# Optimization experiments

Hardware: AMD Instinct MI355X
Metric: run time of the kernel (lower is better)

## Reference

```python
import jax, jax.numpy as jnp
import numpy as np

N_RADIAL = 5
N_BASIS = 7
R_MAX = 6.0
R_MIN = 0.5
N_SPECIES = 119
N_ATOMS = 50000
N_EDGES = 1000000


def tril_2d_indices(n):
    return np.array([(i, j) for i in range(n) for j in range(i + 1)], dtype=np.int32)


def tril_3d_indices(n):
    return np.array([(i, j, k) for i in range(n) for j in range(i + 1) for k in range(j + 1)], dtype=np.int32)


TRIL2 = tril_2d_indices(N_RADIAL)  # [15, 2]
TRIL3 = tril_3d_indices(N_RADIAL)  # [35, 3]


def setup_inputs() -> dict:
    key = jax.random.key(0)
    k1, k2, k3, k4 = jax.random.split(key, 4)
    R = jax.random.normal(k1, (N_ATOMS, 3), dtype=jnp.float32) * 1.5
    Z = jax.random.randint(k2, (N_ATOMS,), 0, N_SPECIES, dtype=jnp.int32)
    neighbor_idxs = jax.random.randint(k3, (2, N_EDGES), 0, N_ATOMS, dtype=jnp.int32)
    box = jnp.zeros((3,), dtype=jnp.float32)
    W = jax.random.normal(k4, (N_SPECIES, N_SPECIES, N_RADIAL, N_BASIS), dtype=jnp.float32)
    return {"R": R, "Z": Z, "neighbor_idxs": neighbor_idxs, "box": box, "W": W}


def reference(R, Z, neighbor_idxs, box, W):
    n_atoms = R.shape[0]
    idx_i, idx_j = neighbor_idxs[0], neighbor_idxs[1]
    # free-space displacement (init_box == 0): R[idx_j] - R[idx_i]
    dr_vec = (R[idx_j] - R[idx_i]).astype(jnp.float32)  # [E, 3]
    dr = jnp.sqrt(jnp.sum(dr_vec * dr_vec, axis=-1))    # [E]
    dn = dr_vec / (dr + 1e-5)[:, None]                  # unit directions [E, 3]

    # radial function: Gaussian basis * cosine cutoff, species-pair coefficients
    shifts = R_MIN + (R_MAX - R_MIN) / N_BASIS * jnp.arange(N_BASIS, dtype=jnp.float32)
    betta = float(N_BASIS ** 2) / float(R_MAX ** 2)
    rad_norm = float((2.0 * betta / np.pi) ** 0.25)
    basis = rad_norm * jnp.exp(-betta * (dr[:, None] - shifts) ** 2)  # [E, n_basis]
    cutoff = 0.5 * (jnp.cos(np.pi * dr / R_MAX) + 1.0) * (dr < R_MAX).astype(dr.dtype)
    coeffs = W[Z[idx_i], Z[idx_j]]  # [E, n_radial, n_basis]
    embed_norm = float(1.0 / np.sqrt(N_BASIS))
    radial = jnp.einsum('en,ern->er', basis, coeffs) * cutoff[:, None] * embed_norm  # [E, R]

    # mask padded (self-index) neighbors
    radial = radial * (idx_i != idx_j).astype(radial.dtype)[:, None]

    # geometric moments: scatter-add per-edge rank-0..3 outer products onto atoms
    seg = lambda x: jax.ops.segment_sum(x, idx_j, num_segments=n_atoms)
    m0 = seg(radial)                                           # [A, R]
    m1 = seg(radial[:, :, None] * dn[:, None, :])              # [A, R, 3]
    dn2 = dn[:, None, :, None] * dn[:, None, None, :]          # [E, 1, 3, 3]
    m2 = seg(radial[:, :, None, None] * dn2)                   # [A, R, 3, 3]
    dn3 = dn2[..., None] * dn[:, None, None, None, :]          # [E, 1, 3, 3, 3]
    m3 = seg(radial[:, :, None, None, None] * dn3)             # [A, R, 3, 3, 3]

    contr_0 = m0
    contr_1 = jnp.einsum('ari,asi->rsa', m1, m1)
    contr_2 = jnp.einsum('arij,asij->rsa', m2, m2)
    contr_3 = jnp.einsum('arijk,asijk->rsa', m3, m3)
    contr_4 = jnp.einsum('arij,asik,atjk->rsta', m2, m2, m2)
    contr_5 = jnp.einsum('ari,asj,atij->rsta', m1, m1, m2)
    contr_6 = jnp.einsum('arijk,asijl,atkl->rsta', m3, m3, m2)
    contr_7 = jnp.einsum('arijk,asij,atk->rsta', m3, m2, m1)

    i2, j2 = TRIL2[:, 0], TRIL2[:, 1]
    i3, j3, k3 = TRIL3[:, 0], TRIL3[:, 1], TRIL3[:, 2]
    n_symm01 = TRIL2.shape[0] * N_RADIAL  # 75

    c1 = jnp.transpose(contr_1[i2, j2])                                    # [A, 15]
    c2 = jnp.transpose(contr_2[i2, j2])                                    # [A, 15]
    c3 = jnp.transpose(contr_3[i2, j2])                                    # [A, 15]
    c4 = jnp.transpose(contr_4[i3, j3, k3])                                # [A, 35]
    c5 = jnp.transpose(jnp.reshape(contr_5[i2, j2], (n_symm01, -1)))       # [A, 75]
    c6 = jnp.transpose(jnp.reshape(contr_6[i2, j2], (n_symm01, -1)))       # [A, 75]
    c7 = jnp.transpose(jnp.reshape(contr_7, (N_RADIAL ** 3, -1)))          # [A, 125]

    return jnp.concatenate([contr_0, c1, c2, c3, c4, c5, c6, c7], axis=-1)  # [A, 360]
```

## Files before the change

kernel.cpp:

```cpp
#include <hip/hip_runtime.h>
#include <cstdint>
#include <cstddef>

#define CAP 48
#define NSP 119
#define CPAD 16

__device__ constexpr int IDX2[9]  = {0,1,2, 1,3,4, 2,4,5};
__device__ constexpr int IDX3[27] = {0,1,2, 1,3,4, 2,4,5,
                                     1,3,4, 3,6,7, 4,7,8,
                                     2,4,5, 4,7,8, 5,8,9};
__device__ constexpr int PR2[15] = {0,1,1,2,2,2,3,3,3,3,4,4,4,4,4};
__device__ constexpr int PS2[15] = {0,0,1,0,1,2,0,1,2,3,0,1,2,3,4};
__device__ constexpr int CB4[15] = {50,51,52,54,55,57,60,61,63,66,70,71,73,76,80};

__global__ __launch_bounds__(256) void prep_kernel(
    const float* __restrict__ R, const int* __restrict__ Z,
    const float* __restrict__ W,
    int* __restrict__ cnt, float4* __restrict__ RZ, float* __restrict__ Wp,
    int n_atoms, int n_wel)
{
    int t = blockIdx.x * blockDim.x + threadIdx.x;
    if (t < n_atoms) {
        cnt[t * CPAD] = 0;
        RZ[t] = make_float4(R[3*t], R[3*t+1], R[3*t+2], __int_as_float(Z[t]));
    }
    if (t < n_wel) {
        int rc = t / 36;
        int u  = t - rc * 36;
        Wp[t] = (u < 35) ? W[rc * 35 + u] : 0.f;
    }
}

__global__ __launch_bounds__(256) void edge_light_kernel(
    const int* __restrict__ nbr, const float4* __restrict__ RZ,
    int* __restrict__ cnt, float4* __restrict__ pay2, int n_edges)
{
    int e = blockIdx.x * blockDim.x + threadIdx.x;
    if (e >= n_edges) return;
    int i = nbr[e];
    int j = nbr[n_edges + e];
    if (i == j) return;
    float4 rzi = RZ[i];
    float4 rzj = RZ[j];
    float dx = rzj.x - rzi.x, dy = rzj.y - rzi.y, dz = rzj.z - rzi.z;
    float dr2 = dx*dx + dy*dy + dz*dz;
    if (!(dr2 < 36.0f)) return;

    int pos = atomicAdd(&cnt[j * CPAD], 1);
    if (pos < CAP) {
        pay2[((size_t)j * CAP + pos) * 2] = make_float4(dx, dy, dz, rzi.w);
    }
}

__global__ __launch_bounds__(192) void expand_kernel(
    const int* __restrict__ Z,
    const int* __restrict__ cnt, float4* __restrict__ pay2,
    const float4* __restrict__ Wp4, int n_atoms)
{
    int tid = threadIdx.x;
    int a    = blockIdx.x * 4 + tid / CAP;
    int slot = tid % CAP;
    if (a >= n_atoms) return;
    int cn = cnt[a * CPAD]; if (cn > CAP) cn = CAP;
    if (slot >= cn) return;

    size_t idx = (size_t)a * CAP + slot;
    float4 q = pay2[2 * idx];
    float dr = sqrtf(q.x*q.x + q.y*q.y + q.z*q.z);
    float inv = 1.0f / (dr + 1e-5f);

    const float betta      = 49.0f/36.0f;
    const float rad_norm   = 0.96481270f;
    const float embed_norm = 0.37796447f;
    const float PI_F       = 3.14159265358979f;
    float cut = 0.5f * (__cosf(PI_F * dr * (1.0f/6.0f)) + 1.0f) * rad_norm * embed_norm;

    float basis[7];
    #pragma unroll
    for (int n = 0; n < 7; n++) {
        float d = dr - (0.5f + (5.5f/7.0f) * (float)n);
        basis[n] = __expf(-betta * d * d);
    }

    int zi = __float_as_int(q.w);
    int za = Z[a];
    int base4 = (zi * NSP + za) * 9;

    float rad[5] = {0,0,0,0,0};
    #pragma unroll
    for (int qq = 0; qq < 9; qq++) {
        float4 wq = Wp4[base4 + qq];
        #pragma unroll
        for (int c = 0; c < 4; c++) {
            int f = 4*qq + c;
            if (f < 35) {
                float wv = (c==0) ? wq.x : (c==1) ? wq.y : (c==2) ? wq.z : wq.w;
                rad[f/7] += basis[f%7] * wv;
            }
        }
    }
    pay2[2*idx    ] = make_float4(q.x*inv, q.y*inv, q.z*inv, rad[4]*cut);
    pay2[2*idx + 1] = make_float4(rad[0]*cut, rad[1]*cut, rad[2]*cut, rad[3]*cut);
}

__global__ __launch_bounds__(256) void scatter_bins_kernel(
    const int* __restrict__ nbr, int* __restrict__ cnt,
    int* __restrict__ bins, int n_edges)
{
    int e = blockIdx.x * blockDim.x + threadIdx.x;
    if (e >= n_edges) return;
    int i = nbr[e];
    int j = nbr[n_edges + e];
    if (i == j) return;
    int pos = atomicAdd(&cnt[j], 1);
    if (pos < CAP) bins[(size_t)j * CAP + pos] = i;
}

__device__ __forceinline__ void edge_math_raw(
    float dx, float dy, float dz, int zi, int za,
    const float4* __restrict__ Wp4, float rv[5], float dn[3])
{
    float dr = sqrtf(dx*dx + dy*dy + dz*dz);
    float inv = 1.0f / (dr + 1e-5f);
    dn[0] = dx*inv; dn[1] = dy*inv; dn[2] = dz*inv;

    const float betta      = 49.0f/36.0f;
    const float rad_norm   = 0.96481270f;
    const float embed_norm = 0.37796447f;
    const float PI_F       = 3.14159265358979f;
    float cut = 0.5f * (__cosf(PI_F * dr * (1.0f/6.0f)) + 1.0f) * rad_norm * embed_norm;

    float basis[7];
    #pragma unroll
    for (int n = 0; n < 7; n++) {
        float d = dr - (0.5f + (5.5f/7.0f) * (float)n);
        basis[n] = __expf(-betta * d * d);
    }

    int base4 = (zi * NSP + za) * 9;
    float rad[5] = {0,0,0,0,0};
    #pragma unroll
    for (int q = 0; q < 9; q++) {
        float4 wq = Wp4[base4 + q];
        #pragma unroll
        for (int c = 0; c < 4; c++) {
            int f = 4*q + c;
            if (f < 35) {
                float wv = (c==0) ? wq.x : (c==1) ? wq.y : (c==2) ? wq.z : wq.w;
                rad[f/7] += basis[f%7] * wv;
            }
        }
    }
    #pragma unroll
    for (int r = 0; r < 5; r++) rv[r] = rad[r] * cut;
}

__device__ __forceinline__ void c6_range(const float* m, float* o, int plo, int phi) {
    for (int p = plo; p < phi; p++) {
        int r = PR2[p], s = PS2[p];
        const float* m3r = m + 50 + r * 10;
        const float* m3s = m + 50 + s * 10;
        float A[3][3] = {{0,0,0},{0,0,0},{0,0,0}};
        #pragma unroll
        for (int i = 0; i < 3; i++)
            #pragma unroll
            for (int j = 0; j < 3; j++)
                #pragma unroll
                for (int k = 0; k < 3; k++)
                    #pragma unroll
                    for (int l = 0; l < 3; l++)
                        A[k][l] += m3r[IDX3[(i*3+j)*3+k]] * m3s[IDX3[(i*3+j)*3+l]];
        int col = 160 + p * 5;
        for (int t = 0; t < 5; t++) {
            const float* m2t = m + 20 + t * 6;
            float acc = 0.f;
            #pragma unroll
            for (int k = 0; k < 3; k++)
                #pragma unroll
                for (int l = 0; l < 3; l++)
                    acc += A[k][l] * m2t[IDX2[k*3+l]];
            o[col + t] = acc;
        }
    }
}

__device__ __forceinline__ void c4_range(const float* m, float* o, int plo, int phi) {
    for (int p = plo; p < phi; p++) {
        int r = PR2[p], s = PS2[p];
        const float* m2r = m + 20 + r * 6;
        const float* m2s = m + 20 + s * 6;
        float B[3][3] = {{0,0,0},{0,0,0},{0,0,0}};
        #pragma unroll
        for (int i = 0; i < 3; i++)
            #pragma unroll
            for (int j = 0; j < 3; j++)
                #pragma unroll
                for (int k = 0; k < 3; k++)
                    B[j][k] += m2r[IDX2[i*3+j]] * m2s[IDX2[i*3+k]];
        int col = CB4[p];
        for (int t = 0; t <= s; t++) {
            const float* m2t = m + 20 + t * 6;
            float acc = 0.f;
            #pragma unroll
            for (int j = 0; j < 3; j++)
                #pragma unroll
                for (int k = 0; k < 3; k++)
                    acc += B[j][k] * m2t[IDX2[j*3+k]];
            o[col + t] = acc;
        }
    }
}

__device__ __forceinline__ void c5_range(const float* m, float* o, int plo, int phi) {
    for (int p = plo; p < phi; p++) {
        int r = PR2[p], s = PS2[p];
        const float* m1r = m + 5 + r * 3;
        const float* m1s = m + 5 + s * 3;
        float P[3][3];
        #pragma unroll
        for (int i = 0; i < 3; i++)
            #pragma unroll
            for (int j = 0; j < 3; j++)
                P[i][j] = m1r[i] * m1s[j];
        int col = 85 + p * 5;
        for (int t = 0; t < 5; t++) {
            const float* m2t = m + 20 + t * 6;
            float acc = 0.f;
            #pragma unroll
            for (int i = 0; i < 3; i++)
                #pragma unroll
                for (int j = 0; j < 3; j++)
                    acc += P[i][j] * m2t[IDX2[i*3+j]];
            o[col + t] = acc;
        }
    }
}

__device__ __forceinline__ void c7_all(const float* m, float* o) {
    for (int r = 0; r < 5; r++) {
        const float* m3r = m + 50 + r * 10;
        for (int s = 0; s < 5; s++) {
            const float* m2s = m + 20 + s * 6;
            float v[3] = {0,0,0};
            #pragma unroll
            for (int i = 0; i < 3; i++)
                #pragma unroll
                for (int j = 0; j < 3; j++)
                    #pragma unroll
                    for (int k = 0; k < 3; k++)
                        v[k] += m3r[IDX3[(i*3+j)*3+k]] * m2s[IDX2[i*3+j]];
            int col = 235 + (r * 5 + s) * 5;
            for (int t = 0; t < 5; t++) {
                const float* m1t = m + 5 + t * 3;
                o[col + t] = v[0]*m1t[0] + v[1]*m1t[1] + v[2]*m1t[2];
            }
        }
    }
}

__device__ __forceinline__ void c0123(const float* m, float* o) {
    for (int r = 0; r < 5; r++) o[r] = m[r];
    const float W2[6]  = {1,2,2,1,2,1};
    const float W3[10] = {1,3,3,3,6,3,1,3,3,1};
    int c1 = 5, c2 = 20, c3 = 35;
    for (int r = 0; r < 5; r++) {
        const float* a1r = m + 5 + r * 3;
        const float* a2r = m + 20 + r * 6;
        const float* a3r = m + 50 + r * 10;
        for (int s = 0; s <= r; s++) {
            const float* a1s = m + 5 + s * 3;
            const float* a2s = m + 20 + s * 6;
            const float* a3s = m + 50 + s * 10;
            float d1 = 0.f, d2 = 0.f, d3 = 0.f;
            #pragma unroll
            for (int u = 0; u < 3; u++)  d1 += a1r[u] * a1s[u];
            #pragma unroll
            for (int u = 0; u < 6; u++)  d2 += W2[u] * a2r[u] * a2s[u];
            #pragma unroll
            for (int u = 0; u < 10; u++) d3 += W3[u] * a3r[u] * a3s[u];
            o[c1++] = d1; o[c2++] = d2; o[c3++] = d3;
        }
    }
}

__device__ __forceinline__ void contract_4wave(
    float sm[64][101], int lane, int w, int a0, int n_atoms, float* __restrict__ out)
{
    int aa = a0 + lane;
    if (aa < n_atoms) {
        const float* m = sm[lane];
        float* o = out + (size_t)aa * 360;
        if (w == 0) {
            c6_range(m, o, 0, 10);
        } else if (w == 1) {
            c6_range(m, o, 10, 15);
            c4_range(m, o, 0, 7);
        } else if (w == 2) {
            c4_range(m, o, 7, 15);
            c5_range(m, o, 0, 15);
        } else {
            c7_all(m, o);
            c0123(m, o);
        }
    }
}

__device__ __forceinline__ void moments_to_out(
    float acc[100], float sm[64][101], int tid, int a0, int n_atoms,
    float* __restrict__ out)
{
    #pragma unroll
    for (int u = 0; u < 100; u++) {
        acc[u] += __shfl_xor(acc[u], 1);
        acc[u] += __shfl_xor(acc[u], 2);
    }
    int g  = tid >> 2;
    int l4 = tid & 3;
    if (a0 + g < n_atoms && l4 == 0) {
        #pragma unroll
        for (int u = 0; u < 100; u++) sm[g][u] = acc[u];
    }
    __syncthreads();
    contract_4wave(sm, tid & 63, tid >> 6, a0, n_atoms, out);
}

__device__ __forceinline__ void accum_edge(float acc[100], const float rv[5], const float dn1[3])
{
    float p2[6] = {dn1[0]*dn1[0], dn1[0]*dn1[1], dn1[0]*dn1[2],
                   dn1[1]*dn1[1], dn1[1]*dn1[2], dn1[2]*dn1[2]};
    float p3[10] = {p2[0]*dn1[0], p2[0]*dn1[1], p2[0]*dn1[2],
                    p2[1]*dn1[1], p2[1]*dn1[2], p2[2]*dn1[2],
                    p2[3]*dn1[1], p2[3]*dn1[2], p2[4]*dn1[2],
                    p2[5]*dn1[2]};
    #pragma unroll
    for (int r = 0; r < 5; r++) {
        float rvv = rv[r];
        acc[r] += rvv;
        #pragma unroll
        for (int u = 0; u < 3; u++)  acc[5  + r*3  + u] += rvv * dn1[u];
        #pragma unroll
        for (int u = 0; u < 6; u++)  acc[20 + r*6  + u] += rvv * p2[u];
        #pragma unroll
        for (int u = 0; u < 10; u++) acc[50 + r*10 + u] += rvv * p3[u];
    }
}

__global__ __launch_bounds__(256) void accum_slot_kernel(
    const int* __restrict__ cnt, const float4* __restrict__ pay2,
    float* __restrict__ out, int n_atoms)
{
    __shared__ float sm[64][101];
    int tid = threadIdx.x;
    int a0  = blockIdx.x * 64;
    int g   = tid >> 2;
    int l4  = tid & 3;
    int a   = a0 + g;

    float acc[100];
    #pragma unroll
    for (int u = 0; u < 100; u++) acc[u] = 0.f;

    if (a < n_atoms) {
        int cn = cnt[a * CPAD]; if (cn > CAP) cn = CAP;
        const float4* row = pay2 + (size_t)a * CAP * 2;
        for (int es = l4; es < cn; es += 4) {
            float4 q1 = row[2*es    ];
            float4 q2 = row[2*es + 1];
            float dn1[3] = {q1.x, q1.y, q1.z};
            float rv[5]  = {q2.x, q2.y, q2.z, q2.w, q1.w};
            accum_edge(acc, rv, dn1);
        }
    }
    moments_to_out(acc, sm, tid, a0, n_atoms, out);
}

__global__ __launch_bounds__(256) void accum_gather_kernel(
    const float4* __restrict__ RZ, const float4* __restrict__ Wp4,
    const int* __restrict__ cnt, const int* __restrict__ bins,
    float* __restrict__ out, int n_atoms)
{
    __shared__ float sm[64][101];
    int tid = threadIdx.x;
    int a0  = blockIdx.x * 64;
    int g   = tid >> 2;
    int l4  = tid & 3;
    int a   = a0 + g;

    float acc[100];
    #pragma unroll
    for (int u = 0; u < 100; u++) acc[u] = 0.f;

    if (a < n_atoms) {
        int cn = cnt[a]; if (cn > CAP) cn = CAP;
        float4 rza = RZ[a];
        int za = __float_as_int(rza.w);
        for (int e = l4; e < cn; e += 4) {
            int i = bins[(size_t)a * CAP + e];
            float4 rzi = RZ[i];
            float dx = rza.x - rzi.x, dy = rza.y - rzi.y, dz = rza.z - rzi.z;
            float dr2 = dx*dx + dy*dy + dz*dz;
            if (!(dr2 < 36.0f)) continue;
            int zi = __float_as_int(rzi.w);
            float rv[5], dn1[3];
            edge_math_raw(dx, dy, dz, zi, za, Wp4, rv, dn1);
            accum_edge(acc, rv, dn1);
        }
    }
    moments_to_out(acc, sm, tid, a0, n_atoms, out);
}

extern "C" void kernel_launch(void* const* d_in, const int* in_sizes, int n_in,
                              void* d_out, int out_size, void* d_ws, size_t ws_size,
                              hipStream_t stream)
{
    const float* R   = (const float*)d_in[0];
    const int*   Z   = (const int*)d_in[1];
    const int*   nbr = (const int*)d_in[2];
    const float* W   = (const float*)d_in[4];
    float* out = (float*)d_out;

    int n_atoms = in_sizes[0] / 3;
    int n_edges = in_sizes[2] / 2;
    int n_wel   = NSP * NSP * 36;

    char* ws = (char*)d_ws;

    size_t szCntPad = (size_t)n_atoms * CPAD * 4;
    size_t szRZ     = (size_t)n_atoms * 16;
    size_t szWp     = (size_t)n_wel * 4;
    size_t szPay2   = (size_t)n_atoms * CAP * 32;
    size_t szIdx    = (size_t)n_atoms * CAP * 4;

    size_t needMain = szCntPad + szPay2 + szRZ + szWp;

    if (ws_size >= needMain) {
        int*    cnt  = (int*)ws;
        float4* pay2 = (float4*)(ws + szCntPad);
        float4* RZ   = (float4*)(ws + szCntPad + szPay2);
        float4* Wp4  = (float4*)(ws + szCntPad + szPay2 + szRZ);

        int prep_n = (n_wel > n_atoms) ? n_wel : n_atoms;
        prep_kernel<<<(prep_n + 255)/256, 256, 0, stream>>>(
            R, Z, W, cnt, RZ, (float*)Wp4, n_atoms, n_wel);
        edge_light_kernel<<<(n_edges + 255)/256, 256, 0, stream>>>(
            nbr, RZ, cnt, pay2, n_edges);
        expand_kernel<<<(n_atoms + 3)/4, 192, 0, stream>>>(
            Z, cnt, pay2, Wp4, n_atoms);
        accum_slot_kernel<<<(n_atoms + 63)/64, 256, 0, stream>>>(
            cnt, pay2, out, n_atoms);
    } else {
        int*    cnt  = (int*)ws;
        int*    bins = (int*)(ws + 204800);
        float4* RZ   = (float4*)(ws + 204800 + szIdx);
        float4* Wp4  = (float4*)(ws + 204800 + szIdx + szRZ);

        hipMemsetAsync(cnt, 0, (size_t)n_atoms * 4, stream);
        prep_kernel<<<(n_wel + 255)/256, 256, 0, stream>>>(
            R, Z, W, cnt, RZ, (float*)Wp4, 0 , n_wel);
        {
            struct Local {
                static __global__ void dummy() {}
            };
        }
        prep_kernel<<<(n_atoms + 255)/256, 256, 0, stream>>>(
            R, Z, W, cnt, RZ, (float*)Wp4, n_atoms, 0);
        scatter_bins_kernel<<<(n_edges + 255)/256, 256, 0, stream>>>(nbr, cnt, bins, n_edges);
        accum_gather_kernel<<<(n_atoms + 63)/64, 256, 0, stream>>>(
            RZ, Wp4, cnt, bins, out, n_atoms);
    }
}
```

Measured before the change: 128.6 us.

## Stage contraction outputs in shared memory for coalesced row stores

The contraction phase now writes each 90-column chunk of the 360-wide output row into a shared-memory buffer, then the whole block stores it cooperatively with consecutive threads writing consecutive addresses. Previously each lane wrote its own atom's row directly, giving strided, uncoalesced global stores. Work is also rebalanced across the four waves per chunk. The cost is extra shared memory (about 23 KB more per block, which may reduce occupancy) and eight extra block barriers.

```diff
diff --git a/kernel.cpp b/kernel.cpp
--- a/kernel.cpp
+++ b/kernel.cpp
@@ -237,24 +237,23 @@
     }
 }
 
-__device__ __forceinline__ void c7_all(const float* m, float* o) {
-    for (int r = 0; r < 5; r++) {
+__device__ __forceinline__ void c7_range(const float* m, float* o, int rs_lo, int rs_hi) {
+    for (int rs = rs_lo; rs < rs_hi; rs++) {
+        int r = rs / 5, s = rs - 5 * (rs / 5);
         const float* m3r = m + 50 + r * 10;
-        for (int s = 0; s < 5; s++) {
-            const float* m2s = m + 20 + s * 6;
-            float v[3] = {0,0,0};
-            #pragma unroll
-            for (int i = 0; i < 3; i++)
-                #pragma unroll
-                for (int j = 0; j < 3; j++)
-                    #pragma unroll
-                    for (int k = 0; k < 3; k++)
-                        v[k] += m3r[IDX3[(i*3+j)*3+k]] * m2s[IDX2[i*3+j]];
-            int col = 235 + (r * 5 + s) * 5;
-            for (int t = 0; t < 5; t++) {
-                const float* m1t = m + 5 + t * 3;
-                o[col + t] = v[0]*m1t[0] + v[1]*m1t[1] + v[2]*m1t[2];
-            }
+        const float* m2s = m + 20 + s * 6;
+        float v[3] = {0,0,0};
+        #pragma unroll
+        for (int i = 0; i < 3; i++)
+            #pragma unroll
+            for (int j = 0; j < 3; j++)
+                #pragma unroll
+                for (int k = 0; k < 3; k++)
+                    v[k] += m3r[IDX3[(i*3+j)*3+k]] * m2s[IDX2[i*3+j]];
+        int col = 235 + rs * 5;
+        for (int t = 0; t < 5; t++) {
+            const float* m1t = m + 5 + t * 3;
+            o[col + t] = v[0]*m1t[0] + v[1]*m1t[1] + v[2]*m1t[2];
         }
     }
 }
@@ -284,31 +283,55 @@
     }
 }
 
-__device__ __forceinline__ void contract_4wave(
-    float sm[64][101], int lane, int w, int a0, int n_atoms, float* __restrict__ out)
-{
-    int aa = a0 + lane;
-    if (aa < n_atoms) {
-        const float* m = sm[lane];
-        float* o = out + (size_t)aa * 360;
-        if (w == 0) {
-            c6_range(m, o, 0, 10);
-        } else if (w == 1) {
-            c6_range(m, o, 10, 15);
-            c4_range(m, o, 0, 7);
-        } else if (w == 2) {
-            c4_range(m, o, 7, 15);
-            c5_range(m, o, 0, 15);
-        } else {
-            c7_all(m, o);
-            c0123(m, o);
-        }
+__device__ __forceinline__ void contract_staged(
+    float sm[64][101], float outbuf[64][91],
+    int tid, int a0, int n_atoms, float* __restrict__ out)
+{
+    int lane = tid & 63;
+    int w    = tid >> 6;
+    int aa   = a0 + lane;
+    bool valid = (aa < n_atoms);
+    const float* m = sm[lane];
+
+    #pragma unroll
+    for (int chunk = 0; chunk < 4; chunk++) {
+        float* o = &outbuf[lane][0] - chunk * 90;
+        if (valid) {
+            if (chunk == 0) {
+                if      (w == 0) c4_range(m, o, 0, 15);
+                else if (w == 1) c0123(m, o);
+                else if (w == 2) c5_range(m, o, 0, 1);
+            } else if (chunk == 1) {
+                if      (w == 0) c6_range(m, o, 0, 2);
+                else if (w == 1) c6_range(m, o, 2, 4);
+                else if (w == 2) c5_range(m, o, 1, 8);
+                else             c5_range(m, o, 8, 15);
+            } else if (chunk == 2) {
+                if      (w == 0) c6_range(m, o, 4, 8);
+                else if (w == 1) c6_range(m, o, 8, 11);
+                else if (w == 2) c6_range(m, o, 11, 15);
+                else             c7_range(m, o, 0, 7);
+            } else {
+                if      (w == 0) c7_range(m, o, 7, 12);
+                else if (w == 1) c7_range(m, o, 12, 16);
+                else if (w == 2) c7_range(m, o, 16, 21);
+                else             c7_range(m, o, 21, 25);
+            }
+        }
+        __syncthreads();
+        for (int idx = tid; idx < 64 * 90; idx += 256) {
+            int row = idx / 90;
+            int col = idx - row * 90;
+            if (a0 + row < n_atoms)
+                out[(size_t)(a0 + row) * 360 + chunk * 90 + col] = outbuf[row][col];
+        }
+        __syncthreads();
     }
 }
 
 __device__ __forceinline__ void moments_to_out(
-    float acc[100], float sm[64][101], int tid, int a0, int n_atoms,
-    float* __restrict__ out)
+    float acc[100], float sm[64][101], float outbuf[64][91],
+    int tid, int a0, int n_atoms, float* __restrict__ out)
 {
     #pragma unroll
     for (int u = 0; u < 100; u++) {
@@ -322,7 +345,7 @@
         for (int u = 0; u < 100; u++) sm[g][u] = acc[u];
     }
     __syncthreads();
-    contract_4wave(sm, tid & 63, tid >> 6, a0, n_atoms, out);
+    contract_staged(sm, outbuf, tid, a0, n_atoms, out);
 }
 
 __device__ __forceinline__ void accum_edge(float acc[100], const float rv[5], const float dn1[3])
@@ -351,6 +374,7 @@
     float* __restrict__ out, int n_atoms)
 {
     __shared__ float sm[64][101];
+    __shared__ float outbuf[64][91];
     int tid = threadIdx.x;
     int a0  = blockIdx.x * 64;
     int g   = tid >> 2;
@@ -372,7 +396,7 @@
             accum_edge(acc, rv, dn1);
         }
     }
-    moments_to_out(acc, sm, tid, a0, n_atoms, out);
+    moments_to_out(acc, sm, outbuf, tid, a0, n_atoms, out);
 }
 
 __global__ __launch_bounds__(256) void accum_gather_kernel(
@@ -381,6 +405,7 @@
     float* __restrict__ out, int n_atoms)
 {
     __shared__ float sm[64][101];
+    __shared__ float outbuf[64][91];
     int tid = threadIdx.x;
     int a0  = blockIdx.x * 64;
     int g   = tid >> 2;
@@ -407,7 +432,7 @@
             accum_edge(acc, rv, dn1);
         }
     }
-    moments_to_out(acc, sm, tid, a0, n_atoms, out);
+    moments_to_out(acc, sm, outbuf, tid, a0, n_atoms, out);
 }
 
 extern "C" void kernel_launch(void* const* d_in, const int* in_sizes, int n_in,
@@ -455,14 +480,9 @@
         float4* RZ   = (float4*)(ws + 204800 + szIdx);
         float4* Wp4  = (float4*)(ws + 204800 + szIdx + szRZ);
 
-        hipMemsetAsync(cnt, 0, (size_t)n_atoms * 4, stream);
+        (void)hipMemsetAsync(cnt, 0, (size_t)n_atoms * 4, stream);
         prep_kernel<<<(n_wel + 255)/256, 256, 0, stream>>>(
-            R, Z, W, cnt, RZ, (float*)Wp4, 0 , n_wel);
-        {
-            struct Local {
-                static __global__ void dummy() {}
-            };
-        }
+            R, Z, W, cnt, RZ, (float*)Wp4, 0, n_wel);
         prep_kernel<<<(n_atoms + 255)/256, 256, 0, stream>>>(
             R, Z, W, cnt, RZ, (float*)Wp4, n_atoms, 0);
         scatter_bins_kernel<<<(n_edges + 255)/256, 256, 0, stream>>>(nbr, cnt, bins, n_edges);
```

Result: slower. 146.7 us (+14.1%).
